# Kernel optimization log

Measured on AMD Instinct MI355X. Metric: run time of the kernel, lower is better.

## Reference

```python
import jax, jax.numpy as jnp
import numpy as np

FP4_AMAX = 6.0
FP8_AMAX = 448.0
E2M1_LUT = jnp.array([0.0, 0.5, 1.0, 1.5, 2.0, 3.0, 4.0, 6.0], dtype=jnp.float32)
# (threshold, code) pairs; applied in order, alternating <= and < comparisons
THRESHOLDS = [(5.0, 6), (3.5, 5), (2.5, 4), (1.75, 3), (1.25, 2), (0.75, 1), (0.25, 0)]


def _fp4_code(a):
    # a: abs-values, float32. Round-to-e2m1 magnitude code per the torch threshold table.
    code = jnp.full(a.shape, 7, dtype=jnp.int32)
    for i, (m, c) in enumerate(THRESHOLDS):
        mask = (a <= m) if i % 2 == 0 else (a < m)
        code = jnp.where(mask, c, code)
    return code


def simulate_nvfp4_quantize(w):
    # w: (out, in), in % 16 == 0. Returns fake-quantized weight, same shape/dtype.
    out_f, in_f = w.shape
    wb = w.reshape(out_f, in_f // 16, 16).astype(jnp.float32)
    gs = (FP4_AMAX * FP8_AMAX) / jnp.max(jnp.abs(wb))          # global fp32 scale
    s_decb = jnp.max(jnp.abs(wb), axis=-1) / FP4_AMAX           # per-16-block decode scale
    xs = jnp.clip(s_decb * gs, -FP8_AMAX, FP8_AMAX).astype(jnp.float8_e4m3fn)  # fp8 block scales
    xs_f = xs.astype(jnp.float32)
    s_encb = gs / jnp.clip(xs_f, 1e-12, None)                   # encode scale per block
    x_scaled = wb * s_encb[..., None]
    sign = jnp.where(jnp.signbit(x_scaled), -1.0, 1.0)
    mag = E2M1_LUT[_fp4_code(jnp.abs(x_scaled))]
    wq = sign * mag * (xs_f / gs)[..., None]                    # dequantize
    return wq.reshape(out_f, in_f).astype(w.dtype)


def setup_inputs() -> dict:
    key = jax.random.key(0)
    k1, k2, k3 = jax.random.split(key, 3)
    B, S, IN, OUT = 4, 2048, 4096, 4096
    x = jax.random.normal(k1, (B, S, IN), dtype=jnp.float32)
    weight = jax.random.normal(k2, (OUT, IN), dtype=jnp.float32) * 0.02
    bias = jax.random.normal(k3, (OUT,), dtype=jnp.float32) * 0.01
    return {"x": x, "weight": weight, "bias": bias}


def reference(x, weight, bias):
    # STE quantization: forward uses fake-quant weight
    weight_q = simulate_nvfp4_quantize(weight)
    # F.linear: x @ W^T + b
    return jnp.einsum("bsi,oi->bso", x, weight_q) + bias
```

## Files before the change

kernel.cpp:

```cpp
#include <hip/hip_runtime.h>
#include <hip/hip_bf16.h>
#include <stdint.h>

typedef __bf16 bf16_t;
typedef __bf16 bf16x8 __attribute__((ext_vector_type(8)));
typedef float  f32x4  __attribute__((ext_vector_type(4)));

#define BM 256
#define BN 256
#define BK 64
#define NTHREADS 512

__global__ void k_absmax(const float* __restrict__ w, unsigned int* __restrict__ out_bits, int n4) {
    int i = blockIdx.x * blockDim.x + threadIdx.x;
    int stride = gridDim.x * blockDim.x;
    const float4* w4 = (const float4*)w;
    float m = 0.0f;
    for (; i < n4; i += stride) {
        float4 v = w4[i];
        m = fmaxf(m, fmaxf(fmaxf(fabsf(v.x), fabsf(v.y)), fmaxf(fabsf(v.z), fabsf(v.w))));
    }
    #pragma unroll
    for (int off = 32; off; off >>= 1)
        m = fmaxf(m, __shfl_xor(m, off));
    if ((threadIdx.x & 63) == 0)
        atomicMax(out_bits, __float_as_uint(m));
}

__device__ __forceinline__ float e4m3_rne(float v) {
    if (v < 0.015625f) {
        return rintf(v * 512.0f) * (1.0f / 512.0f);
    }
    unsigned int u = __float_as_uint(v);
    unsigned int keep = u >> 20;
    unsigned int r = u & 0xFFFFFu;
    if (r > 0x80000u || (r == 0x80000u && (keep & 1u))) keep++;
    return __uint_as_float(keep << 20);
}

__global__ void k_quantize(const float* __restrict__ w, bf16_t* __restrict__ wq,
                           const unsigned int* __restrict__ maxbits, int nblk) {
    int t = blockIdx.x * blockDim.x + threadIdx.x;
    if (t >= nblk) return;
    float gmax = __uint_as_float(*maxbits);
    float gs = 2688.0f / gmax;
    const float4* w4 = (const float4*)w + (size_t)t * 4;
    float4 v0 = w4[0], v1 = w4[1], v2 = w4[2], v3 = w4[3];
    float vv[16];
    vv[0]=v0.x; vv[1]=v0.y; vv[2]=v0.z; vv[3]=v0.w;
    vv[4]=v1.x; vv[5]=v1.y; vv[6]=v1.z; vv[7]=v1.w;
    vv[8]=v2.x; vv[9]=v2.y; vv[10]=v2.z; vv[11]=v2.w;
    vv[12]=v3.x; vv[13]=v3.y; vv[14]=v3.z; vv[15]=v3.w;
    float bmax = 0.0f;
    #pragma unroll
    for (int j = 0; j < 16; ++j) bmax = fmaxf(bmax, fabsf(vv[j]));
    float s_decb = bmax / 6.0f;
    float xs_in  = fminf(s_decb * gs, 448.0f);
    float xs_f   = e4m3_rne(xs_in);
    float s_encb = gs / fmaxf(xs_f, 1e-12f);
    float dscale = xs_f / gs;
    bf16x8 o0, o1;
    #pragma unroll
    for (int j = 0; j < 16; ++j) {
        float xsc = vv[j] * s_encb;
        float a = fabsf(xsc);
        float mag = (a <= 0.25f) ? 0.0f
                  : (a <  0.75f) ? 0.5f
                  : (a <= 1.25f) ? 1.0f
                  : (a <  1.75f) ? 1.5f
                  : (a <= 2.5f ) ? 2.0f
                  : (a <  3.5f ) ? 3.0f
                  : (a <= 5.0f ) ? 4.0f : 6.0f;
        float sgn = __builtin_copysignf(1.0f, xsc);
        float val = (sgn * mag) * dscale;
        if (j < 8) o0[j] = (bf16_t)val; else o1[j - 8] = (bf16_t)val;
    }
    *(bf16x8*)(wq + (size_t)t * 16)     = o0;
    *(bf16x8*)(wq + (size_t)t * 16 + 8) = o1;
}

__global__ void k_cvt_x(const float* __restrict__ x, bf16_t* __restrict__ xb, long n8) {
    long i = blockIdx.x * (long)blockDim.x + threadIdx.x;
    long stride = (long)gridDim.x * blockDim.x;
    const float4* x4 = (const float4*)x;
    for (; i < n8; i += stride) {
        float4 a = x4[2 * i], b = x4[2 * i + 1];
        bf16x8 o;
        o[0] = (bf16_t)a.x; o[1] = (bf16_t)a.y; o[2] = (bf16_t)a.z; o[3] = (bf16_t)a.w;
        o[4] = (bf16_t)b.x; o[5] = (bf16_t)b.y; o[6] = (bf16_t)b.z; o[7] = (bf16_t)b.w;
        *(bf16x8*)(xb + i * 8) = o;
    }
}

__device__ __forceinline__ void BARRIER() {
    asm volatile("" ::: "memory");
    __builtin_amdgcn_s_barrier();
    asm volatile("" ::: "memory");
}

__device__ __forceinline__ void gload16(const bf16_t* g, bf16_t* l) {
    __builtin_amdgcn_global_load_lds(
        (const __attribute__((address_space(1))) unsigned int*)g,
        (__attribute__((address_space(3))) unsigned int*)l,
        16, 0, 0);
}

__device__ __forceinline__ bf16x8 ldsf(const bf16_t* tile, int row, int g) {
    return *(const bf16x8*)(tile + (((row << 3) + (g ^ (row & 7))) << 3));
}

__global__ __launch_bounds__(NTHREADS, 2) void k_gemm(
        const bf16_t* __restrict__ A,
        const bf16_t* __restrict__ Bt,
        const float*  __restrict__ bias,
        float* __restrict__ C, int M, int N, int K) {
    __shared__ __align__(16) bf16_t sA[2][BM * BK];
    __shared__ __align__(16) bf16_t sB[2][BN * BK];

    int bid = blockIdx.x;
    int cpx = gridDim.x >> 3;
    int swz = (bid & 7) * cpx + (bid >> 3);
    int nbn = N / BN;
    int m0 = (swz / nbn) * BM, n0 = (swz % nbn) * BN;

    int tid  = threadIdx.x;
    int lane = tid & 63;
    int w    = tid >> 6;
    int wr   = w >> 2, wc = w & 3;
    int fr   = lane & 15;
    int gk   = lane >> 4;

    int eoff[2][2], loff[2][2];
    #pragma unroll
    for (int H = 0; H < 2; ++H) {
        #pragma unroll
        for (int r = 0; r < 2; ++r) {
            int pf  = H * 1024 + r * 512 + tid;
            int row = pf >> 3;
            int lg  = (pf & 7) ^ (row & 7);
            eoff[H][r] = row * K + lg * 8;
            loff[H][r] = pf * 8;
        }
    }
    const bf16_t* Ab = A  + (size_t)m0 * K;
    const bf16_t* Bb = Bt + (size_t)n0 * K;

#define STAGE(MAT, H, BUF, KK) do {                                          \
        gload16(MAT##b + eoff[H][0] + (KK), &s##MAT[BUF][loff[H][0]]);       \
        gload16(MAT##b + eoff[H][1] + (KK), &s##MAT[BUF][loff[H][1]]);       \
    } while (0)

    f32x4 acc[8][4] = {};

    STAGE(B, 0, 0, 0);  STAGE(B, 1, 0, 0);
    STAGE(A, 0, 0, 0);  STAGE(A, 1, 0, 0);
    STAGE(B, 0, 1, BK); STAGE(B, 1, 1, BK);
    asm volatile("s_waitcnt vmcnt(4)" ::: "memory");
    BARRIER();

    const int NT = K / BK;
    const int rA = wr * 128 + fr;
    const int rB = wc * 64 + fr;

#define PHASE(QM, STAGE_STMT, TAIL_STMT)                                                              \
    {                                                                                                  \
        bf16x8 a00 = ldsf(pA, rA + (QM)*32,      gk);                                                  \
        bf16x8 a01 = ldsf(pA, rA + (QM)*32,      4 + gk);                                              \
        bf16x8 a10 = ldsf(pA, rA + (QM)*32 + 16, gk);                                                  \
        bf16x8 a11 = ldsf(pA, rA + (QM)*32 + 16, 4 + gk);                                              \
        STAGE_STMT;                                                                                    \
        BARRIER();                                                                                     \
        asm volatile("s_waitcnt lgkmcnt(0)" ::: "memory");                                             \
        __builtin_amdgcn_s_setprio(1);                                                                 \
        _Pragma("unroll")                                                                              \
        for (int j = 0; j < 4; ++j) {                                                                  \
            acc[(QM)*2+0][j] = __builtin_amdgcn_mfma_f32_16x16x32_bf16(a00, bfr[j][0], acc[(QM)*2+0][j], 0, 0, 0); \
            acc[(QM)*2+0][j] = __builtin_amdgcn_mfma_f32_16x16x32_bf16(a01, bfr[j][1], acc[(QM)*2+0][j], 0, 0, 0); \
            acc[(QM)*2+1][j] = __builtin_amdgcn_mfma_f32_16x16x32_bf16(a10, bfr[j][0], acc[(QM)*2+1][j], 0, 0, 0); \
            acc[(QM)*2+1][j] = __builtin_amdgcn_mfma_f32_16x16x32_bf16(a11, bfr[j][1], acc[(QM)*2+1][j], 0, 0, 0); \
        }                                                                                              \
        __builtin_amdgcn_s_setprio(0);                                                                 \
        TAIL_STMT;                                                                                     \
        BARRIER();                                                                                     \
    }

    for (int t = 0; t < NT; ++t) {
        int cur = t & 1;
        const bf16_t* pA = sA[cur];
        const bf16_t* pB = sB[cur];
        int ktA = ((t + 1 < NT) ? t + 1 : NT - 1) * BK;
        int ktB = ((t + 2 < NT) ? t + 2 : NT - 1) * BK;
        int bA = cur ^ 1, bB = cur;

        bf16x8 bfr[4][2];
        #pragma unroll
        for (int j = 0; j < 4; ++j) {
            bfr[j][0] = ldsf(pB, rB + j * 16, gk);
            bfr[j][1] = ldsf(pB, rB + j * 16, 4 + gk);
        }

        PHASE(0, STAGE(A, 0, bA, ktA), (void)0);
        PHASE(1, STAGE(A, 1, bA, ktA), (void)0);
        PHASE(2, STAGE(B, 0, bB, ktB), (void)0);
        PHASE(3, STAGE(B, 1, bB, ktB),
              asm volatile("s_waitcnt vmcnt(4)" ::: "memory"));
    }
    asm volatile("s_waitcnt vmcnt(0)" ::: "memory");

    int crow = (lane >> 4) * 4;
    int ccol = lane & 15;
    float bv[4];
    #pragma unroll
    for (int j = 0; j < 4; ++j) bv[j] = bias[n0 + wc * 64 + j * 16 + ccol];
    #pragma unroll
    for (int i = 0; i < 8; ++i) {
        size_t mrow = (size_t)(m0 + wr * 128 + i * 16 + crow);
        #pragma unroll
        for (int j = 0; j < 4; ++j) {
            float* cp = C + mrow * N + (n0 + wc * 64 + j * 16 + ccol);
            #pragma unroll
            for (int r = 0; r < 4; ++r)
                cp[(size_t)r * N] = acc[i][j][r] + bv[j];
        }
    }
#undef PHASE
#undef STAGE
}

extern "C" void kernel_launch(void* const* d_in, const int* in_sizes, int n_in,
                              void* d_out, int out_size, void* d_ws, size_t ws_size,
                              hipStream_t stream) {
    const float* x    = (const float*)d_in[0];
    const float* wgt  = (const float*)d_in[1];
    const float* bias = (const float*)d_in[2];
    float* out = (float*)d_out;

    const int N = in_sizes[2];
    const int K = in_sizes[1] / N;
    const int M = in_sizes[0] / K;

    unsigned int* maxbits = (unsigned int*)d_ws;
    bf16_t* wq = (bf16_t*)((char*)d_ws + 256);
    bf16_t* xb = (bf16_t*)((char*)d_ws + 256 + (size_t)N * K * sizeof(bf16_t));

    hipMemsetAsync(d_ws, 0, 256, stream);
    k_absmax<<<512, 256, 0, stream>>>(wgt, maxbits, N * K / 4);
    int nblk = N * K / 16;
    k_quantize<<<(nblk + 255) / 256, 256, 0, stream>>>(wgt, wq, maxbits, nblk);
    long n8 = (long)M * K / 8;
    k_cvt_x<<<2048, 256, 0, stream>>>(x, xb, n8);
    dim3 grid((M / BM) * (N / BN));
    k_gemm<<<grid, NTHREADS, 0, stream>>>(xb, wq, bias, out, M, N, K);
}
```

Baseline: 348.5 us.

## Software-pipeline LDS fragment loads with ping-pong A registers across MFMA groups

Restructures the GEMM main loop so each group's A fragments are loaded from LDS while the previous group's MFMAs run, using two ping-pong register sets (afA/afB). The B fragments for the next k-tile are prefetched inside the last MFMA group, and the A fragments for the next tile are loaded before the loop iteration ends. Barriers are reduced from two per phase to one, and the vmcnt wait is moved. The aim is to hide LDS latency and barrier stalls behind matrix math, at the cost of higher register pressure and subtler LDS read/write ordering between buffers.

```diff
diff --git a/kernel.cpp b/kernel.cpp
--- a/kernel.cpp
+++ b/kernel.cpp
@@ -150,7 +150,25 @@
         gload16(MAT##b + eoff[H][1] + (KK), &s##MAT[BUF][loff[H][1]]);       \
     } while (0)
 
+#define MFMA_GROUP(Q, AF)                                                                             \
+    do {                                                                                              \
+        __builtin_amdgcn_s_setprio(1);                                                                \
+        _Pragma("unroll")                                                                             \
+        for (int j = 0; j < 4; ++j) {                                                                 \
+            acc[(Q)*2+0][j] = __builtin_amdgcn_mfma_f32_16x16x32_bf16(AF[0], bfr[j][0], acc[(Q)*2+0][j], 0, 0, 0); \
+            acc[(Q)*2+0][j] = __builtin_amdgcn_mfma_f32_16x16x32_bf16(AF[1], bfr[j][1], acc[(Q)*2+0][j], 0, 0, 0); \
+            acc[(Q)*2+1][j] = __builtin_amdgcn_mfma_f32_16x16x32_bf16(AF[2], bfr[j][0], acc[(Q)*2+1][j], 0, 0, 0); \
+            acc[(Q)*2+1][j] = __builtin_amdgcn_mfma_f32_16x16x32_bf16(AF[3], bfr[j][1], acc[(Q)*2+1][j], 0, 0, 0); \
+        }                                                                                             \
+        __builtin_amdgcn_s_setprio(0);                                                                \
+    } while (0)
+
     f32x4 acc[8][4] = {};
+    bf16x8 afA[4], afB[4], bfr[4][2];
+
+    const int NT = K / BK;
+    const int rA = wr * 128 + fr;
+    const int rB = wc * 64 + fr;
 
     STAGE(B, 0, 0, 0);  STAGE(B, 1, 0, 0);
     STAGE(A, 0, 0, 0);  STAGE(A, 1, 0, 0);
@@ -158,52 +176,61 @@
     asm volatile("s_waitcnt vmcnt(4)" ::: "memory");
     BARRIER();
 
-    const int NT = K / BK;
-    const int rA = wr * 128 + fr;
-    const int rB = wc * 64 + fr;
-
-#define PHASE(QM, STAGE_STMT, TAIL_STMT)                                                              \
-    {                                                                                                  \
-        bf16x8 a00 = ldsf(pA, rA + (QM)*32,      gk);                                                  \
-        bf16x8 a01 = ldsf(pA, rA + (QM)*32,      4 + gk);                                              \
-        bf16x8 a10 = ldsf(pA, rA + (QM)*32 + 16, gk);                                                  \
-        bf16x8 a11 = ldsf(pA, rA + (QM)*32 + 16, 4 + gk);                                              \
-        STAGE_STMT;                                                                                    \
-        BARRIER();                                                                                     \
-        asm volatile("s_waitcnt lgkmcnt(0)" ::: "memory");                                             \
-        __builtin_amdgcn_s_setprio(1);                                                                 \
-        _Pragma("unroll")                                                                              \
-        for (int j = 0; j < 4; ++j) {                                                                  \
-            acc[(QM)*2+0][j] = __builtin_amdgcn_mfma_f32_16x16x32_bf16(a00, bfr[j][0], acc[(QM)*2+0][j], 0, 0, 0); \
-            acc[(QM)*2+0][j] = __builtin_amdgcn_mfma_f32_16x16x32_bf16(a01, bfr[j][1], acc[(QM)*2+0][j], 0, 0, 0); \
-            acc[(QM)*2+1][j] = __builtin_amdgcn_mfma_f32_16x16x32_bf16(a10, bfr[j][0], acc[(QM)*2+1][j], 0, 0, 0); \
-            acc[(QM)*2+1][j] = __builtin_amdgcn_mfma_f32_16x16x32_bf16(a11, bfr[j][1], acc[(QM)*2+1][j], 0, 0, 0); \
-        }                                                                                              \
-        __builtin_amdgcn_s_setprio(0);                                                                 \
-        TAIL_STMT;                                                                                     \
-        BARRIER();                                                                                     \
-    }
+    #pragma unroll
+    for (int j = 0; j < 4; ++j) {
+        bfr[j][0] = ldsf(sB[0], rB + j * 16, gk);
+        bfr[j][1] = ldsf(sB[0], rB + j * 16, 4 + gk);
+    }
+    afA[0] = ldsf(sA[0], rA,      gk);  afA[1] = ldsf(sA[0], rA,      4 + gk);
+    afA[2] = ldsf(sA[0], rA + 16, gk);  afA[3] = ldsf(sA[0], rA + 16, 4 + gk);
 
     for (int t = 0; t < NT; ++t) {
-        int cur = t & 1;
-        const bf16_t* pA = sA[cur];
-        const bf16_t* pB = sB[cur];
-        int ktA = ((t + 1 < NT) ? t + 1 : NT - 1) * BK;
-        int ktB = ((t + 2 < NT) ? t + 2 : NT - 1) * BK;
-        int bA = cur ^ 1, bB = cur;
-
-        bf16x8 bfr[4][2];
+        const int cur = t & 1;
+        const bf16_t* pA  = sA[cur];
+        const bf16_t* pAn = sA[cur ^ 1];
+        const bf16_t* pBn = sB[cur ^ 1];
+        int ktA = ((t + 1 < NT) ? t + 1 : t) * BK;
+        int ktB = ((t + 2 < NT) ? t + 2 : t) * BK;
+        const int bA = cur ^ 1, bB = cur;
+
+        afB[0] = ldsf(pA, rA + 32, gk);  afB[1] = ldsf(pA, rA + 32, 4 + gk);
+        afB[2] = ldsf(pA, rA + 48, gk);  afB[3] = ldsf(pA, rA + 48, 4 + gk);
+        STAGE(A, 0, bA, ktA);
+        asm volatile("" ::: "memory");
+        MFMA_GROUP(0, afA);
+        BARRIER();
+
+        afA[0] = ldsf(pA, rA + 64, gk);  afA[1] = ldsf(pA, rA + 64, 4 + gk);
+        afA[2] = ldsf(pA, rA + 80, gk);  afA[3] = ldsf(pA, rA + 80, 4 + gk);
+        STAGE(A, 1, bA, ktA);
+        asm volatile("" ::: "memory");
+        MFMA_GROUP(1, afB);
+        BARRIER();
+
+        afB[0] = ldsf(pA, rA + 96,  gk);  afB[1] = ldsf(pA, rA + 96,  4 + gk);
+        afB[2] = ldsf(pA, rA + 112, gk);  afB[3] = ldsf(pA, rA + 112, 4 + gk);
+        STAGE(B, 0, bB, ktB);
+        asm volatile("" ::: "memory");
+        MFMA_GROUP(2, afA);
+        asm volatile("s_waitcnt vmcnt(2)" ::: "memory");
+        BARRIER();
+
+        afA[0] = ldsf(pAn, rA,      gk);  afA[1] = ldsf(pAn, rA,      4 + gk);
+        afA[2] = ldsf(pAn, rA + 16, gk);  afA[3] = ldsf(pAn, rA + 16, 4 + gk);
+        STAGE(B, 1, bB, ktB);
+        asm volatile("" ::: "memory");
+        __builtin_amdgcn_s_setprio(1);
         #pragma unroll
         for (int j = 0; j < 4; ++j) {
-            bfr[j][0] = ldsf(pB, rB + j * 16, gk);
-            bfr[j][1] = ldsf(pB, rB + j * 16, 4 + gk);
+            acc[6][j] = __builtin_amdgcn_mfma_f32_16x16x32_bf16(afB[0], bfr[j][0], acc[6][j], 0, 0, 0);
+            acc[6][j] = __builtin_amdgcn_mfma_f32_16x16x32_bf16(afB[1], bfr[j][1], acc[6][j], 0, 0, 0);
+            acc[7][j] = __builtin_amdgcn_mfma_f32_16x16x32_bf16(afB[2], bfr[j][0], acc[7][j], 0, 0, 0);
+            acc[7][j] = __builtin_amdgcn_mfma_f32_16x16x32_bf16(afB[3], bfr[j][1], acc[7][j], 0, 0, 0);
+            bfr[j][0] = ldsf(pBn, rB + j * 16, gk);
+            bfr[j][1] = ldsf(pBn, rB + j * 16, 4 + gk);
         }
-
-        PHASE(0, STAGE(A, 0, bA, ktA), (void)0);
-        PHASE(1, STAGE(A, 1, bA, ktA), (void)0);
-        PHASE(2, STAGE(B, 0, bB, ktB), (void)0);
-        PHASE(3, STAGE(B, 1, bB, ktB),
-              asm volatile("s_waitcnt vmcnt(4)" ::: "memory"));
+        __builtin_amdgcn_s_setprio(0);
+        BARRIER();
     }
     asm volatile("s_waitcnt vmcnt(0)" ::: "memory");
 
@@ -223,7 +250,7 @@
                 cp[(size_t)r * N] = acc[i][j][r] + bv[j];
         }
     }
-#undef PHASE
+#undef MFMA_GROUP
 #undef STAGE
 }
 
```

Result: no change. 351.5 us (+0.9%).

## Restructure GEMM main loop into unrolled two-tile pipeline with new LDS swizzle

Applied to the files above, without the earlier changes.

Rewrites the bf16 MFMA GEMM main loop: each iteration now handles two K tiles with static buffer indices. Global-to-LDS stage loads are rescheduled so the next A half-tile and upcoming B tiles are in flight deeper ahead. The LDS swizzle changes to a new XOR pattern with precomputed base offsets, and a partial lgkmcnt wait is added after the B fragment reads. The goal is to remove per-iteration address math and branching and to hide global latency better. In exchange the loop assumes an even tile count and the vmcnt accounting is more fragile.

```diff
diff --git a/kernel.cpp b/kernel.cpp
--- a/kernel.cpp
+++ b/kernel.cpp
@@ -105,10 +105,6 @@
         16, 0, 0);
 }
 
-__device__ __forceinline__ bf16x8 ldsf(const bf16_t* tile, int row, int g) {
-    return *(const bf16x8*)(tile + (((row << 3) + (g ^ (row & 7))) << 3));
-}
-
 __global__ __launch_bounds__(NTHREADS, 2) void k_gemm(
         const bf16_t* __restrict__ A,
         const bf16_t* __restrict__ Bt,
@@ -127,83 +123,145 @@
     int lane = tid & 63;
     int w    = tid >> 6;
     int wr   = w >> 2, wc = w & 3;
-    int fr   = lane & 15;
-    int gk   = lane >> 4;
-
-    int eoff[2][2], loff[2][2];
-    #pragma unroll
-    for (int H = 0; H < 2; ++H) {
-        #pragma unroll
-        for (int r = 0; r < 2; ++r) {
-            int pf  = H * 1024 + r * 512 + tid;
-            int row = pf >> 3;
-            int lg  = (pf & 7) ^ (row & 7);
-            eoff[H][r] = row * K + lg * 8;
-            loff[H][r] = pf * 8;
-        }
+    int fr15 = lane & 15;
+    int kg   = lane >> 4;
+
+    int rowin = (tid >> 3) & 63;
+    int pg    = tid & 7;
+    int gsw   = pg ^ (rowin & 7);
+    int gstg[2], lstg[2];
+    #pragma unroll
+    for (int l = 0; l < 2; ++l) {
+        gstg[l] = (l * 128 + rowin) * K + gsw * 8;
+        lstg[l] = (l * 128 + rowin) * 64 + pg * 8;
     }
     const bf16_t* Ab = A  + (size_t)m0 * K;
     const bf16_t* Bb = Bt + (size_t)n0 * K;
 
-#define STAGE(MAT, H, BUF, KK) do {                                          \
-        gload16(MAT##b + eoff[H][0] + (KK), &s##MAT[BUF][loff[H][0]]);       \
-        gload16(MAT##b + eoff[H][1] + (KK), &s##MAT[BUF][loff[H][1]]);       \
+#define STG(SX, Xb, BUF, H, KT) do {                                              \
+        gload16(Xb + (H) * 64 * K + gstg[0] + (KT), &SX[BUF][(H) * 4096 + lstg[0]]); \
+        gload16(Xb + (H) * 64 * K + gstg[1] + (KT), &SX[BUF][(H) * 4096 + lstg[1]]); \
     } while (0)
 
+    int f01 = fr15 & 3, f2 = (fr15 >> 2) & 1;
+    int pgr0 = 4 * (0 ^ f2) + (kg ^ f01);
+    int pgr1 = 4 * (1 ^ f2) + (kg ^ f01);
+    int baseA0 = (wr * 128 + fr15) * 64 + pgr0 * 8;
+    int baseA1 = (wr * 128 + fr15) * 64 + pgr1 * 8;
+    int baseB0 = (wc * 64  + fr15) * 64 + pgr0 * 8;
+    int baseB1 = (wc * 64  + fr15) * 64 + pgr1 * 8;
+
     f32x4 acc[8][4] = {};
-
-    STAGE(B, 0, 0, 0);  STAGE(B, 1, 0, 0);
-    STAGE(A, 0, 0, 0);  STAGE(A, 1, 0, 0);
-    STAGE(B, 0, 1, BK); STAGE(B, 1, 1, BK);
-    asm volatile("s_waitcnt vmcnt(4)" ::: "memory");
+    bf16x8 bfr[4][2];
+
+    const int NT = K / BK;
+    const int ITERS = NT / 2;
+
+    STG(sB, Bb, 0, 0, 0);  STG(sB, Bb, 0, 1, 0);
+    STG(sA, Ab, 0, 0, 0);  STG(sA, Ab, 0, 1, 0);
+    STG(sB, Bb, 1, 0, BK); STG(sB, Bb, 1, 1, BK);
+    STG(sA, Ab, 1, 0, BK);
+    asm volatile("s_waitcnt vmcnt(6)" ::: "memory");
     BARRIER();
 
-    const int NT = K / BK;
-    const int rA = wr * 128 + fr;
-    const int rB = wc * 64 + fr;
-
-#define PHASE(QM, STAGE_STMT, TAIL_STMT)                                                              \
-    {                                                                                                  \
-        bf16x8 a00 = ldsf(pA, rA + (QM)*32,      gk);                                                  \
-        bf16x8 a01 = ldsf(pA, rA + (QM)*32,      4 + gk);                                              \
-        bf16x8 a10 = ldsf(pA, rA + (QM)*32 + 16, gk);                                                  \
-        bf16x8 a11 = ldsf(pA, rA + (QM)*32 + 16, 4 + gk);                                              \
-        STAGE_STMT;                                                                                    \
-        BARRIER();                                                                                     \
-        asm volatile("s_waitcnt lgkmcnt(0)" ::: "memory");                                             \
-        __builtin_amdgcn_s_setprio(1);                                                                 \
-        _Pragma("unroll")                                                                              \
-        for (int j = 0; j < 4; ++j) {                                                                  \
-            acc[(QM)*2+0][j] = __builtin_amdgcn_mfma_f32_16x16x32_bf16(a00, bfr[j][0], acc[(QM)*2+0][j], 0, 0, 0); \
-            acc[(QM)*2+0][j] = __builtin_amdgcn_mfma_f32_16x16x32_bf16(a01, bfr[j][1], acc[(QM)*2+0][j], 0, 0, 0); \
-            acc[(QM)*2+1][j] = __builtin_amdgcn_mfma_f32_16x16x32_bf16(a10, bfr[j][0], acc[(QM)*2+1][j], 0, 0, 0); \
-            acc[(QM)*2+1][j] = __builtin_amdgcn_mfma_f32_16x16x32_bf16(a11, bfr[j][1], acc[(QM)*2+1][j], 0, 0, 0); \
-        }                                                                                              \
-        __builtin_amdgcn_s_setprio(0);                                                                 \
-        TAIL_STMT;                                                                                     \
-        BARRIER();                                                                                     \
-    }
-
-    for (int t = 0; t < NT; ++t) {
-        int cur = t & 1;
-        const bf16_t* pA = sA[cur];
-        const bf16_t* pB = sB[cur];
-        int ktA = ((t + 1 < NT) ? t + 1 : NT - 1) * BK;
-        int ktB = ((t + 2 < NT) ? t + 2 : NT - 1) * BK;
-        int bA = cur ^ 1, bB = cur;
-
-        bf16x8 bfr[4][2];
-        #pragma unroll
-        for (int j = 0; j < 4; ++j) {
-            bfr[j][0] = ldsf(pB, rB + j * 16, gk);
-            bfr[j][1] = ldsf(pB, rB + j * 16, 4 + gk);
-        }
-
-        PHASE(0, STAGE(A, 0, bA, ktA), (void)0);
-        PHASE(1, STAGE(A, 1, bA, ktA), (void)0);
-        PHASE(2, STAGE(B, 0, bB, ktB), (void)0);
-        PHASE(3, STAGE(B, 1, bB, ktB),
-              asm volatile("s_waitcnt vmcnt(4)" ::: "memory"));
+#define RDA(PA, Q, A0K0, A0K1, A1K0, A1K1)                                \
+    bf16x8 A0K0 = *(const bf16x8*)((PA) + baseA0 + (Q) * 2048);            \
+    bf16x8 A0K1 = *(const bf16x8*)((PA) + baseA1 + (Q) * 2048);            \
+    bf16x8 A1K0 = *(const bf16x8*)((PA) + baseA0 + (Q) * 2048 + 1024);     \
+    bf16x8 A1K1 = *(const bf16x8*)((PA) + baseA1 + (Q) * 2048 + 1024);
+
+#define RDB(PB) do {                                                       \
+        _Pragma("unroll")                                                  \
+        for (int j = 0; j < 4; ++j) {                                      \
+            bfr[j][0] = *(const bf16x8*)((PB) + baseB0 + j * 1024);        \
+            bfr[j][1] = *(const bf16x8*)((PB) + baseB1 + j * 1024);        \
+        }                                                                  \
+    } while (0)
+
+#define MF16(Q, A0K0, A0K1, A1K0, A1K1) do {                                                       \
+        __builtin_amdgcn_s_setprio(1);                                                             \
+        _Pragma("unroll")                                                                          \
+        for (int j = 0; j < 4; ++j) {                                                              \
+            acc[(Q)*2+0][j] = __builtin_amdgcn_mfma_f32_16x16x32_bf16(A0K0, bfr[j][0], acc[(Q)*2+0][j], 0, 0, 0); \
+            acc[(Q)*2+0][j] = __builtin_amdgcn_mfma_f32_16x16x32_bf16(A0K1, bfr[j][1], acc[(Q)*2+0][j], 0, 0, 0); \
+            acc[(Q)*2+1][j] = __builtin_amdgcn_mfma_f32_16x16x32_bf16(A1K0, bfr[j][0], acc[(Q)*2+1][j], 0, 0, 0); \
+            acc[(Q)*2+1][j] = __builtin_amdgcn_mfma_f32_16x16x32_bf16(A1K1, bfr[j][1], acc[(Q)*2+1][j], 0, 0, 0); \
+        }                                                                                          \
+        __builtin_amdgcn_s_setprio(0);                                                             \
+    } while (0)
+
+#define LGKM0() asm volatile("s_waitcnt lgkmcnt(0)" ::: "memory")
+#define LGKM8() asm volatile("s_waitcnt lgkmcnt(8)" ::: "memory")
+
+    for (int it = 0; it < ITERS; ++it) {
+        const bool nl = (it + 1 < ITERS);
+        const int ktP = (2 * it + 1) * BK;
+        const int kt2 = (2 * it + 2) * BK;
+        const int kt3 = (2 * it + 3) * BK;
+
+        {
+            RDA(sA[0], 0, a00, a01, a10, a11);
+            RDB(sB[0]);
+            STG(sA, Ab, 1, 1, ktP);
+            LGKM8();
+            BARRIER(); LGKM0();
+            MF16(0, a00, a01, a10, a11);
+            BARRIER();
+        }
+        {
+            RDA(sA[0], 1, a00, a01, a10, a11);
+            if (nl) STG(sB, Bb, 0, 0, kt2);
+            BARRIER(); LGKM0();
+            MF16(1, a00, a01, a10, a11);
+            BARRIER();
+        }
+        {
+            RDA(sA[0], 2, a00, a01, a10, a11);
+            if (nl) STG(sB, Bb, 0, 1, kt2);
+            BARRIER(); LGKM0();
+            MF16(2, a00, a01, a10, a11);
+            BARRIER();
+        }
+        {
+            RDA(sA[0], 3, a00, a01, a10, a11);
+            if (nl) STG(sA, Ab, 0, 0, kt2);
+            BARRIER(); LGKM0();
+            MF16(3, a00, a01, a10, a11);
+            if (nl) { asm volatile("s_waitcnt vmcnt(6)" ::: "memory"); }
+            else    { asm volatile("s_waitcnt vmcnt(0)" ::: "memory"); }
+            BARRIER();
+        }
+        {
+            RDA(sA[1], 0, a00, a01, a10, a11);
+            RDB(sB[1]);
+            if (nl) STG(sA, Ab, 0, 1, kt2);
+            LGKM8();
+            BARRIER(); LGKM0();
+            MF16(0, a00, a01, a10, a11);
+            BARRIER();
+        }
+        {
+            RDA(sA[1], 1, a00, a01, a10, a11);
+            if (nl) STG(sB, Bb, 1, 0, kt3);
+            BARRIER(); LGKM0();
+            MF16(1, a00, a01, a10, a11);
+            BARRIER();
+        }
+        {
+            RDA(sA[1], 2, a00, a01, a10, a11);
+            if (nl) STG(sB, Bb, 1, 1, kt3);
+            BARRIER(); LGKM0();
+            MF16(2, a00, a01, a10, a11);
+            BARRIER();
+        }
+        {
+            RDA(sA[1], 3, a00, a01, a10, a11);
+            if (nl) STG(sA, Ab, 1, 0, kt3);
+            BARRIER(); LGKM0();
+            MF16(3, a00, a01, a10, a11);
+            if (nl) { asm volatile("s_waitcnt vmcnt(6)" ::: "memory"); }
+            BARRIER();
+        }
     }
     asm volatile("s_waitcnt vmcnt(0)" ::: "memory");
 
@@ -223,8 +281,12 @@
                 cp[(size_t)r * N] = acc[i][j][r] + bv[j];
         }
     }
-#undef PHASE
-#undef STAGE
+#undef STG
+#undef RDA
+#undef RDB
+#undef MF16
+#undef LGKM0
+#undef LGKM8
 }
 
 extern "C" void kernel_launch(void* const* d_in, const int* in_sizes, int n_in,
```

Measured after the change: 336.0 us. -3.6%, faster.

## Restructure GEMM main loop into 8-phase ping-pong schedule with quadrant MFMA blocks

Applied to the files above, without the earlier changes.

Rewrites the bf16 GEMM main loop to process two K-tiles per iteration in eight phases. Each phase reads a 4x2 fragment quadrant from LDS and issues 16 MFMAs. Global-to-LDS staging is interleaved at a finer granularity across both buffers, and the LDS swizzle layout and staging offsets change. The goal is better overlap of global loads, LDS reads and MFMA work with fewer stalls per barrier, at the cost of more barriers, more complex vmcnt accounting and possible register pressure from holding A and B fragments.

```diff
diff --git a/kernel.cpp b/kernel.cpp
--- a/kernel.cpp
+++ b/kernel.cpp
@@ -105,10 +105,6 @@
         16, 0, 0);
 }
 
-__device__ __forceinline__ bf16x8 ldsf(const bf16_t* tile, int row, int g) {
-    return *(const bf16x8*)(tile + (((row << 3) + (g ^ (row & 7))) << 3));
-}
-
 __global__ __launch_bounds__(NTHREADS, 2) void k_gemm(
         const bf16_t* __restrict__ A,
         const bf16_t* __restrict__ Bt,
@@ -127,83 +123,136 @@
     int lane = tid & 63;
     int w    = tid >> 6;
     int wr   = w >> 2, wc = w & 3;
-    int fr   = lane & 15;
-    int gk   = lane >> 4;
-
-    int eoff[2][2], loff[2][2];
-    #pragma unroll
-    for (int H = 0; H < 2; ++H) {
-        #pragma unroll
-        for (int r = 0; r < 2; ++r) {
-            int pf  = H * 1024 + r * 512 + tid;
-            int row = pf >> 3;
-            int lg  = (pf & 7) ^ (row & 7);
-            eoff[H][r] = row * K + lg * 8;
-            loff[H][r] = pf * 8;
-        }
+    int fr15 = lane & 15;
+    int kg   = lane >> 4;
+
+    int rowin = tid >> 3;
+    int pg    = tid & 7;
+    int gsw   = pg ^ (rowin & 7);
+    int gstg[2], lstg[2];
+    #pragma unroll
+    for (int l = 0; l < 2; ++l) {
+        gstg[l] = (l * 128 + rowin) * K + gsw * 8;
+        lstg[l] = (l * 128 + rowin) * 64 + pg * 8;
+    }
+    int tq0 = tid >> 8;
+    int rB  = (tid >> 3) & 31;
+    int gbstg[2], lbstg[2];
+    #pragma unroll
+    for (int l = 0; l < 2; ++l) {
+        int q = l * 2 + tq0;
+        gbstg[l] = (q * 64 + rB) * K + gsw * 8;
+        lbstg[l] = (q * 64 + rB) * 64 + pg * 8;
     }
     const bf16_t* Ab = A  + (size_t)m0 * K;
     const bf16_t* Bb = Bt + (size_t)n0 * K;
 
-#define STAGE(MAT, H, BUF, KK) do {                                          \
-        gload16(MAT##b + eoff[H][0] + (KK), &s##MAT[BUF][loff[H][0]]);       \
-        gload16(MAT##b + eoff[H][1] + (KK), &s##MAT[BUF][loff[H][1]]);       \
-    } while (0)
+#define STGA(BUF, H, KT) do {                                                      \
+        gload16(Ab + (H) * 64 * K + gstg[0] + (KT), &sA[BUF][(H) * 4096 + lstg[0]]); \
+        gload16(Ab + (H) * 64 * K + gstg[1] + (KT), &sA[BUF][(H) * 4096 + lstg[1]]); \
+    } while (0)
+#define STGB(BUF, H, KT) do {                                                      \
+        gload16(Bb + (H) * 32 * K + gbstg[0] + (KT), &sB[BUF][(H) * 2048 + lbstg[0]]); \
+        gload16(Bb + (H) * 32 * K + gbstg[1] + (KT), &sB[BUF][(H) * 2048 + lbstg[1]]); \
+    } while (0)
+
+    int f01 = fr15 & 3, f2 = (fr15 >> 2) & 1;
+    int pgr0 = 4 * (0 ^ f2) + (kg ^ f01);
+    int pgr1 = 4 * (1 ^ f2) + (kg ^ f01);
+    int baseA0 = (wr * 128 + fr15) * 64 + pgr0 * 8;
+    int baseA1 = (wr * 128 + fr15) * 64 + pgr1 * 8;
+    int baseB0 = (wc * 64  + fr15) * 64 + pgr0 * 8;
+    int baseB1 = (wc * 64  + fr15) * 64 + pgr1 * 8;
 
     f32x4 acc[8][4] = {};
-
-    STAGE(B, 0, 0, 0);  STAGE(B, 1, 0, 0);
-    STAGE(A, 0, 0, 0);  STAGE(A, 1, 0, 0);
-    STAGE(B, 0, 1, BK); STAGE(B, 1, 1, BK);
-    asm volatile("s_waitcnt vmcnt(4)" ::: "memory");
+    bf16x8 afr[4][2];
+    bf16x8 bfr[4][2];
+
+    const int NT = K / BK;
+    const int ITERS = NT / 2;
+
+    STGB(0, 0, 0);  STGB(0, 1, 0);
+    STGA(0, 0, 0);  STGA(0, 1, 0);
+    STGB(1, 0, BK); STGB(1, 1, BK);
+    STGA(1, 0, BK);
+    asm volatile("s_waitcnt vmcnt(6)" ::: "memory");
     BARRIER();
 
-    const int NT = K / BK;
-    const int rA = wr * 128 + fr;
-    const int rB = wc * 64 + fr;
-
-#define PHASE(QM, STAGE_STMT, TAIL_STMT)                                                              \
-    {                                                                                                  \
-        bf16x8 a00 = ldsf(pA, rA + (QM)*32,      gk);                                                  \
-        bf16x8 a01 = ldsf(pA, rA + (QM)*32,      4 + gk);                                              \
-        bf16x8 a10 = ldsf(pA, rA + (QM)*32 + 16, gk);                                                  \
-        bf16x8 a11 = ldsf(pA, rA + (QM)*32 + 16, 4 + gk);                                              \
-        STAGE_STMT;                                                                                    \
-        BARRIER();                                                                                     \
-        asm volatile("s_waitcnt lgkmcnt(0)" ::: "memory");                                             \
-        __builtin_amdgcn_s_setprio(1);                                                                 \
-        _Pragma("unroll")                                                                              \
-        for (int j = 0; j < 4; ++j) {                                                                  \
-            acc[(QM)*2+0][j] = __builtin_amdgcn_mfma_f32_16x16x32_bf16(a00, bfr[j][0], acc[(QM)*2+0][j], 0, 0, 0); \
-            acc[(QM)*2+0][j] = __builtin_amdgcn_mfma_f32_16x16x32_bf16(a01, bfr[j][1], acc[(QM)*2+0][j], 0, 0, 0); \
-            acc[(QM)*2+1][j] = __builtin_amdgcn_mfma_f32_16x16x32_bf16(a10, bfr[j][0], acc[(QM)*2+1][j], 0, 0, 0); \
-            acc[(QM)*2+1][j] = __builtin_amdgcn_mfma_f32_16x16x32_bf16(a11, bfr[j][1], acc[(QM)*2+1][j], 0, 0, 0); \
-        }                                                                                              \
-        __builtin_amdgcn_s_setprio(0);                                                                 \
-        TAIL_STMT;                                                                                     \
-        BARRIER();                                                                                     \
-    }
-
-    for (int t = 0; t < NT; ++t) {
-        int cur = t & 1;
-        const bf16_t* pA = sA[cur];
-        const bf16_t* pB = sB[cur];
-        int ktA = ((t + 1 < NT) ? t + 1 : NT - 1) * BK;
-        int ktB = ((t + 2 < NT) ? t + 2 : NT - 1) * BK;
-        int bA = cur ^ 1, bB = cur;
-
-        bf16x8 bfr[4][2];
-        #pragma unroll
-        for (int j = 0; j < 4; ++j) {
-            bfr[j][0] = ldsf(pB, rB + j * 16, gk);
-            bfr[j][1] = ldsf(pB, rB + j * 16, 4 + gk);
-        }
-
-        PHASE(0, STAGE(A, 0, bA, ktA), (void)0);
-        PHASE(1, STAGE(A, 1, bA, ktA), (void)0);
-        PHASE(2, STAGE(B, 0, bB, ktB), (void)0);
-        PHASE(3, STAGE(B, 1, bB, ktB),
-              asm volatile("s_waitcnt vmcnt(4)" ::: "memory"));
+#define RDA4(PA, MH) do {                                                          \
+        _Pragma("unroll")                                                          \
+        for (int m = 0; m < 4; ++m) {                                              \
+            afr[m][0] = *(const bf16x8*)((PA) + baseA0 + ((MH) * 4 + m) * 1024);   \
+            afr[m][1] = *(const bf16x8*)((PA) + baseA1 + ((MH) * 4 + m) * 1024);   \
+        }                                                                          \
+    } while (0)
+
+#define RDB2(PB, NH) do {                                                          \
+        _Pragma("unroll")                                                          \
+        for (int j = 0; j < 2; ++j) {                                              \
+            bfr[(NH)*2+j][0] = *(const bf16x8*)((PB) + baseB0 + ((NH)*2+j) * 1024);\
+            bfr[(NH)*2+j][1] = *(const bf16x8*)((PB) + baseB1 + ((NH)*2+j) * 1024);\
+        }                                                                          \
+    } while (0)
+
+#define MFQ(MH, NH) do {                                                                            \
+        __builtin_amdgcn_s_setprio(1);                                                              \
+        _Pragma("unroll")                                                                           \
+        for (int n = 0; n < 2; ++n)                                                                 \
+            _Pragma("unroll")                                                                       \
+            for (int m = 0; m < 4; ++m)                                                             \
+                acc[(MH)*4+m][(NH)*2+n] = __builtin_amdgcn_mfma_f32_16x16x32_bf16(                  \
+                    afr[m][0], bfr[(NH)*2+n][0], acc[(MH)*4+m][(NH)*2+n], 0, 0, 0);                 \
+        _Pragma("unroll")                                                                           \
+        for (int n = 0; n < 2; ++n)                                                                 \
+            _Pragma("unroll")                                                                       \
+            for (int m = 0; m < 4; ++m)                                                             \
+                acc[(MH)*4+m][(NH)*2+n] = __builtin_amdgcn_mfma_f32_16x16x32_bf16(                  \
+                    afr[m][1], bfr[(NH)*2+n][1], acc[(MH)*4+m][(NH)*2+n], 0, 0, 0);                 \
+        __builtin_amdgcn_s_setprio(0);                                                              \
+    } while (0)
+
+#define LGKM0() asm volatile("s_waitcnt lgkmcnt(0)" ::: "memory")
+
+    for (int it = 0; it < ITERS; ++it) {
+        const bool nl = (it + 1 < ITERS);
+        const int ktB1 = (2 * it + 1) * BK;
+        const int kt2  = (2 * it + 2) * BK;
+        const int kt3  = (2 * it + 3) * BK;
+
+        RDA4(sA[0], 0); RDB2(sB[0], 0);
+        STGA(1, 1, ktB1);
+        BARRIER(); LGKM0(); MFQ(0, 0); BARRIER();
+
+        RDB2(sB[0], 1);
+        if (nl) STGB(0, 0, kt2);
+        BARRIER(); LGKM0(); MFQ(0, 1); BARRIER();
+
+        RDA4(sA[0], 1);
+        if (nl) STGB(0, 1, kt2);
+        BARRIER(); LGKM0(); MFQ(1, 0); BARRIER();
+
+        if (nl) STGA(0, 0, kt2);
+        BARRIER(); MFQ(1, 1);
+        if (nl) { asm volatile("s_waitcnt vmcnt(6)" ::: "memory"); }
+        else    { asm volatile("s_waitcnt vmcnt(0)" ::: "memory"); }
+        BARRIER();
+
+        RDA4(sA[1], 0); RDB2(sB[1], 0);
+        if (nl) STGA(0, 1, kt2);
+        BARRIER(); LGKM0(); MFQ(0, 0); BARRIER();
+
+        RDB2(sB[1], 1);
+        if (nl) STGB(1, 0, kt3);
+        BARRIER(); LGKM0(); MFQ(0, 1); BARRIER();
+
+        RDA4(sA[1], 1);
+        if (nl) STGB(1, 1, kt3);
+        BARRIER(); LGKM0(); MFQ(1, 0); BARRIER();
+
+        if (nl) STGA(1, 0, kt3);
+        BARRIER(); MFQ(1, 1);
+        if (nl) { asm volatile("s_waitcnt vmcnt(6)" ::: "memory"); }
+        BARRIER();
     }
     asm volatile("s_waitcnt vmcnt(0)" ::: "memory");
 
@@ -223,8 +272,12 @@
                 cp[(size_t)r * N] = acc[i][j][r] + bv[j];
         }
     }
-#undef PHASE
-#undef STAGE
+#undef STGA
+#undef STGB
+#undef RDA4
+#undef RDB2
+#undef MFQ
+#undef LGKM0
 }
 
 extern "C" void kernel_launch(void* const* d_in, const int* in_sizes, int n_in,
```

After: 331.3 us. 1.05x faster.
